# Performance work log

Hardware: AMD Instinct MI355X
Metric: run time of the kernel (lower is better)

Reference implementation:

```python
import jax, jax.numpy as jnp
import numpy as np

NUM_NODES = 50000
NUM_FEATS = 64
NUM_HEADS = 2
NUM_EDGES = 800000


def setup_inputs() -> dict:
    key = jax.random.key(0)
    k1, k2, k3 = jax.random.split(key, 3)
    x = jax.random.normal(k1, (NUM_NODES, NUM_FEATS), dtype=jnp.float32)
    # qk_lin: Linear(num_feats, 2*num_feats*num_heads)
    lim = 1.0 / np.sqrt(NUM_FEATS)
    W_qk = jax.random.uniform(k2, (NUM_FEATS, 2 * NUM_HEADS * NUM_FEATS),
                              dtype=jnp.float32, minval=-lim, maxval=lim)
    b_qk = jnp.zeros((2 * NUM_HEADS * NUM_FEATS,), dtype=jnp.float32)
    edge_index = jax.random.randint(k3, (2, NUM_EDGES), 0, NUM_NODES, dtype=jnp.int32)
    return {"x": x, "W_qk": W_qk, "b_qk": b_qk, "edge_index": edge_index}


def reference(x, W_qk, b_qk, edge_index):
    """Edge-restricted multi-head QK attention with sparse softmax over
    each row's outgoing edges, averaged over heads. Returns per-edge
    attention values [E] (sparse COO values; indices == edge_index)."""
    N, F = x.shape
    H = W_qk.shape[1] // (2 * F)
    # qk: [N, 2*H*F] -> [N, H, 2, F]; q/k split matches einops rearranges
    qk = (x @ W_qk + b_qk).reshape(N, H, 2, F)
    q = qk[:, :, 0, :]  # [N, H, F]
    k = qk[:, :, 1, :]  # [N, H, F]
    row, col = edge_index[0], edge_index[1]
    # per-edge per-head scores: q[row] . k[col]  -> [E, H]
    s = jnp.einsum('ehf,ehf->eh', q[row], k[col])
    # sparse softmax over dim=2 (columns) == segment softmax grouped by row
    m = jax.ops.segment_max(s, row, num_segments=N)      # [N, H]
    ex = jnp.exp(s - m[row])                             # [E, H]
    denom = jax.ops.segment_sum(ex, row, num_segments=N)  # [N, H]
    p = ex / denom[row]                                  # [E, H]
    # torch.sparse.sum over heads / num_heads == mean over heads
    return jnp.mean(p, axis=1)  # [E]
```

## Files before the change

### kernel.cpp

```cpp
#include <hip/hip_runtime.h>
#include <hip/hip_bf16.h>


#define NFEAT 64
#define NCOL  256
#define WT_STRIDE 72

typedef __attribute__((ext_vector_type(8))) short bf16x8;
typedef __attribute__((ext_vector_type(4))) float f32x4;

__device__ __forceinline__ unsigned short f2bf(float f) {
    union { __hip_bfloat16 h; unsigned short u; } cv;
    cv.h = __float2bfloat16(f);
    return cv.u;
}

__device__ __forceinline__ float dot_bf16x2(unsigned a, unsigned b) {
    float alo = __uint_as_float(a << 16), ahi = __uint_as_float(a & 0xFFFF0000u);
    float blo = __uint_as_float(b << 16), bhi = __uint_as_float(b & 0xFFFF0000u);
    return alo * blo + ahi * bhi;
}

__global__ __launch_bounds__(256) void gemm_qk_mfma(
    const float* __restrict__ x, const float* __restrict__ W,
    const float* __restrict__ b,
    unsigned short* __restrict__ qo, unsigned short* __restrict__ ko,
    float* __restrict__ den, int N)
{
    __shared__ unsigned short WtL[NCOL * WT_STRIDE];
    __shared__ float bL[NCOL];
    const int tid = threadIdx.x;

    for (int i = tid; i < NFEAT * NCOL; i += 256) {
        const int kk = i >> 8, c = i & 255;
        WtL[c * WT_STRIDE + kk] = f2bf(W[i]);
    }
    bL[tid] = b[tid];

    const int t = blockIdx.x * 256 + tid;
    if (t < 2 * N) den[t] = 0.f;

    const int lane = tid & 63;
    const int wv   = tid >> 6;
    const int l15  = lane & 15;
    const int quad = lane >> 4;
    const int base = blockIdx.x * 128 + wv * 32;
    __syncthreads();

    if (base >= N) return;

    bf16x8 afrag[2][2];
#pragma unroll
    for (int s = 0; s < 2; ++s) {
        int m = base + s * 16 + l15;
        if (m >= N) m = N - 1;
        const float* xp = x + (size_t)m * NFEAT + quad * 8;
#pragma unroll
        for (int ks = 0; ks < 2; ++ks) {
            float4 a0 = *(const float4*)(xp + ks * 32);
            float4 a1 = *(const float4*)(xp + ks * 32 + 4);
            bf16x8 f;
            f[0] = f2bf(a0.x); f[1] = f2bf(a0.y); f[2] = f2bf(a0.z); f[3] = f2bf(a0.w);
            f[4] = f2bf(a1.x); f[5] = f2bf(a1.y); f[6] = f2bf(a1.z); f[7] = f2bf(a1.w);
            afrag[s][ks] = f;
        }
    }

#pragma unroll 4
    for (int ct = 0; ct < 16; ++ct) {
        const int c = ct * 16 + l15;
        bf16x8 b0 = *(const bf16x8*)(WtL + (size_t)c * WT_STRIDE + quad * 8);
        bf16x8 b1 = *(const bf16x8*)(WtL + (size_t)c * WT_STRIDE + 32 + quad * 8);
        const float bias = bL[c];
        const int h   = c >> 7;
        const int isk = (c >> 6) & 1;
        const int f0  = c & 63;
        unsigned short* dst = isk ? ko : qo;
#pragma unroll
        for (int s = 0; s < 2; ++s) {
            f32x4 acc = {0.f, 0.f, 0.f, 0.f};
            acc = __builtin_amdgcn_mfma_f32_16x16x32_bf16(afrag[s][0], b0, acc, 0, 0, 0);
            acc = __builtin_amdgcn_mfma_f32_16x16x32_bf16(afrag[s][1], b1, acc, 0, 0, 0);
#pragma unroll
            for (int r = 0; r < 4; ++r) {
                const int m = base + s * 16 + quad * 4 + r;
                if (m < N)
                    dst[(size_t)m * 128 + h * 64 + f0] = f2bf(acc[r] + bias);
            }
        }
    }
}

__global__ __launch_bounds__(256) void edge_scores_exp(
    const unsigned short* __restrict__ q, const unsigned short* __restrict__ k,
    const int* __restrict__ ei, float* __restrict__ ex_out,
    float* __restrict__ denom, int E)
{
    const int grp  = (int)((blockIdx.x * 256 + threadIdx.x) >> 4);
    const int lane = threadIdx.x & 15;
    const int g0   = grp * 4;
    if (g0 >= E) return;

    int v = 0;
    if (lane < 4)      v = ei[g0 + lane];
    else if (lane < 8) v = ei[E + g0 + (lane - 4)];
    int rows[4], cols[4];
#pragma unroll
    for (int i = 0; i < 4; ++i) {
        rows[i] = __shfl(v, i, 16);
        cols[i] = __shfl(v, 4 + i, 16);
    }

    uint4 qa[4], ka[4];
#pragma unroll
    for (int i = 0; i < 4; ++i) {
        qa[i] = ((const uint4*)(q + (size_t)rows[i] * 128))[lane];
        ka[i] = ((const uint4*)(k + (size_t)cols[i] * 128))[lane];
    }

#pragma unroll
    for (int i = 0; i < 4; ++i) {
        float p = dot_bf16x2(qa[i].x, ka[i].x) + dot_bf16x2(qa[i].y, ka[i].y)
                + dot_bf16x2(qa[i].z, ka[i].z) + dot_bf16x2(qa[i].w, ka[i].w);
        p += __shfl_xor(p, 1);
        p += __shfl_xor(p, 2);
        p += __shfl_xor(p, 4);
        if ((lane & 7) == 0 && g0 + i < E) {
            const int h  = lane >> 3;
            const float e = __expf(p);
            ex_out[(size_t)(g0 + i) * 2 + h] = e;
            atomicAdd(&denom[(size_t)rows[i] * 2 + h], e);
        }
    }
}

__global__ __launch_bounds__(256) void edge_out_k(
    const int* __restrict__ ei, const float* __restrict__ ex,
    const float* __restrict__ denom, float* __restrict__ out, int E)
{
    const int e = blockIdx.x * 256 + threadIdx.x;
    if (e >= E) return;
    const int row = ei[e];
    const float2 exv = *(const float2*)&ex[(size_t)e * 2];
    const float2 dv  = *(const float2*)&denom[(size_t)row * 2];
    out[e] = 0.5f * (exv.x / dv.x + exv.y / dv.y);
}

extern "C" void kernel_launch(void* const* d_in, const int* in_sizes, int n_in,
                              void* d_out, int out_size, void* d_ws, size_t ws_size,
                              hipStream_t stream)
{
    const float* x   = (const float*)d_in[0];
    const float* W   = (const float*)d_in[1];
    const float* b   = (const float*)d_in[2];
    const int*   ei  = (const int*)d_in[3];
    float*       out = (float*)d_out;

    const int N = in_sizes[0] / NFEAT;
    const int E = in_sizes[3] / 2;

    char* ws = (char*)d_ws;
    size_t off = 0;
    auto alloc = [&](size_t bytes) { void* p = ws + off; off += (bytes + 255) & ~(size_t)255; return p; };
    unsigned short* q_ws  = (unsigned short*)alloc((size_t)N * 128 * 2);
    unsigned short* k_ws  = (unsigned short*)alloc((size_t)N * 128 * 2);
    float*          ex_ws = (float*)alloc((size_t)E * 2 * sizeof(float));
    float*          den_ws= (float*)alloc((size_t)N * 2 * sizeof(float));
    (void)ws_size;

    gemm_qk_mfma<<<(N + 127) / 128, 256, 0, stream>>>(x, W, b, q_ws, k_ws, den_ws, N);
    edge_scores_exp<<<((size_t)(E + 3) / 4 * 16 + 255) / 256, 256, 0, stream>>>(q_ws, k_ws, ei, ex_ws, den_ws, E);
    edge_out_k<<<(E + 255) / 256, 256, 0, stream>>>(ei, ex_ws, den_ws, out, E);
}
```

Baseline: 142.3 us.

## Build CSR by row and compute segment softmax per row without atomics

Replaces the per-edge score kernel, which used atomic denominator accumulation, and the separate normalisation kernel. A histogram, a two-level scan and a scatter now build a row-sorted CSR of (col, edge id). A per-row kernel then computes scores, the exp values and the denominator in registers, and writes normalised outputs. The aim is to remove float atomics and reuse each row's q vector across its edges, at the cost of five extra launches, an integer-atomic scatter and a serial per-row loop with load imbalance from varying degree.

```diff
diff --git a/kernel.cpp b/kernel.cpp
--- a/kernel.cpp
+++ b/kernel.cpp
@@ -24,8 +24,7 @@
 __global__ __launch_bounds__(256) void gemm_qk_mfma(
     const float* __restrict__ x, const float* __restrict__ W,
     const float* __restrict__ b,
-    unsigned short* __restrict__ qo, unsigned short* __restrict__ ko,
-    float* __restrict__ den, int N)
+    unsigned short* __restrict__ qo, unsigned short* __restrict__ ko, int N)
 {
     __shared__ unsigned short WtL[NCOL * WT_STRIDE];
     __shared__ float bL[NCOL];
@@ -36,9 +35,6 @@
         WtL[c * WT_STRIDE + kk] = f2bf(W[i]);
     }
     bL[tid] = b[tid];
-
-    const int t = blockIdx.x * 256 + tid;
-    if (t < 2 * N) den[t] = 0.f;
 
     const int lane = tid & 63;
     const int wv   = tid >> 6;
@@ -91,59 +87,112 @@
     }
 }
 
-__global__ __launch_bounds__(256) void edge_scores_exp(
+__global__ __launch_bounds__(256) void hist_k(const int* __restrict__ ei,
+                                              unsigned* __restrict__ cnt, int E) {
+    const int e = blockIdx.x * 256 + threadIdx.x;
+    if (e < E) atomicAdd(&cnt[ei[e]], 1u);
+}
+
+__global__ __launch_bounds__(256) void scan_a(const unsigned* __restrict__ cnt,
+                                              unsigned* __restrict__ rsl,
+                                              unsigned* __restrict__ bsum, int n) {
+    __shared__ unsigned wsum[4];
+    const int idx  = blockIdx.x * 256 + threadIdx.x;
+    const int lane = threadIdx.x & 63;
+    const int wv   = threadIdx.x >> 6;
+    unsigned v = (idx < n) ? cnt[idx] : 0u;
+    unsigned inc = v;
+    for (int off = 1; off < 64; off <<= 1) {
+        unsigned t = __shfl_up(inc, off, 64);
+        if (lane >= off) inc += t;
+    }
+    if (lane == 63) wsum[wv] = inc;
+    __syncthreads();
+    unsigned wbase = 0;
+    for (int i = 0; i < wv; ++i) wbase += wsum[i];
+    if (idx < n) rsl[idx] = wbase + inc - v;
+    if (threadIdx.x == 255) bsum[blockIdx.x] = wbase + inc;
+}
+
+__global__ __launch_bounds__(256) void scan_b(const unsigned* __restrict__ bsum,
+                                              unsigned* __restrict__ bpre, int nb) {
+    __shared__ unsigned wsum[4];
+    const int t    = threadIdx.x;
+    const int lane = t & 63;
+    const int wv   = t >> 6;
+    unsigned v = (t < nb) ? bsum[t] : 0u;
+    unsigned inc = v;
+    for (int off = 1; off < 64; off <<= 1) {
+        unsigned u = __shfl_up(inc, off, 64);
+        if (lane >= off) inc += u;
+    }
+    if (lane == 63) wsum[wv] = inc;
+    __syncthreads();
+    unsigned wbase = 0;
+    for (int i = 0; i < wv; ++i) wbase += wsum[i];
+    bpre[t] = wbase + inc - v;
+}
+
+__global__ __launch_bounds__(256) void scat_k(const int* __restrict__ ei,
+                                              const unsigned* __restrict__ rsl,
+                                              const unsigned* __restrict__ bpre,
+                                              unsigned* __restrict__ cursor,
+                                              uint2* __restrict__ csr, int E) {
+    const int e = blockIdx.x * 256 + threadIdx.x;
+    if (e >= E) return;
+    const int r = ei[e];
+    const unsigned base = rsl[r] + bpre[r >> 8];
+    const unsigned p = base + atomicAdd(&cursor[r], 1u);
+    csr[p] = make_uint2((unsigned)ei[E + e], (unsigned)e);
+}
+
+__global__ __launch_bounds__(256) void row_k(
     const unsigned short* __restrict__ q, const unsigned short* __restrict__ k,
-    const int* __restrict__ ei, float* __restrict__ ex_out,
-    float* __restrict__ denom, int E)
+    const uint2* __restrict__ csr, const unsigned* __restrict__ rsl,
+    const unsigned* __restrict__ bpre, float* __restrict__ exb,
+    float* __restrict__ out, int N)
 {
     const int grp  = (int)((blockIdx.x * 256 + threadIdx.x) >> 4);
     const int lane = threadIdx.x & 15;
-    const int g0   = grp * 4;
-    if (g0 >= E) return;
-
-    int v = 0;
-    if (lane < 4)      v = ei[g0 + lane];
-    else if (lane < 8) v = ei[E + g0 + (lane - 4)];
-    int rows[4], cols[4];
-#pragma unroll
-    for (int i = 0; i < 4; ++i) {
-        rows[i] = __shfl(v, i, 16);
-        cols[i] = __shfl(v, 4 + i, 16);
-    }
-
-    uint4 qa[4], ka[4];
-#pragma unroll
-    for (int i = 0; i < 4; ++i) {
-        qa[i] = ((const uint4*)(q + (size_t)rows[i] * 128))[lane];
-        ka[i] = ((const uint4*)(k + (size_t)cols[i] * 128))[lane];
-    }
-
-#pragma unroll
-    for (int i = 0; i < 4; ++i) {
-        float p = dot_bf16x2(qa[i].x, ka[i].x) + dot_bf16x2(qa[i].y, ka[i].y)
-                + dot_bf16x2(qa[i].z, ka[i].z) + dot_bf16x2(qa[i].w, ka[i].w);
+    const bool live = (grp < N);
+
+    unsigned start = 0; int deg = 0;
+    uint4 qa = make_uint4(0, 0, 0, 0);
+    if (live) {
+        start = rsl[grp] + bpre[grp >> 8];
+        const unsigned end = rsl[grp + 1] + bpre[(grp + 1) >> 8];
+        deg = (int)(end - start);
+        qa = ((const uint4*)(q + (size_t)grp * 128))[lane];
+    }
+
+    float den0 = 0.f, den1 = 0.f;
+    uint2 pr = (deg > 0) ? csr[start] : make_uint2(0u, 0u);
+    for (int j = 0; j < deg; ++j) {
+        uint2 nx = (j + 1 < deg) ? csr[start + j + 1] : pr;
+        uint4 ka = ((const uint4*)(k + (size_t)pr.x * 128))[lane];
+        float p = dot_bf16x2(qa.x, ka.x) + dot_bf16x2(qa.y, ka.y)
+                + dot_bf16x2(qa.z, ka.z) + dot_bf16x2(qa.w, ka.w);
         p += __shfl_xor(p, 1);
         p += __shfl_xor(p, 2);
         p += __shfl_xor(p, 4);
-        if ((lane & 7) == 0 && g0 + i < E) {
-            const int h  = lane >> 3;
+        if ((lane & 7) == 0) {
             const float e = __expf(p);
-            ex_out[(size_t)(g0 + i) * 2 + h] = e;
-            atomicAdd(&denom[(size_t)rows[i] * 2 + h], e);
+            exb[2 * (size_t)(start + j) + (lane >> 3)] = e;
+            if (lane == 0) den0 += e; else den1 += e;
         }
-    }
-}
-
-__global__ __launch_bounds__(256) void edge_out_k(
-    const int* __restrict__ ei, const float* __restrict__ ex,
-    const float* __restrict__ denom, float* __restrict__ out, int E)
-{
-    const int e = blockIdx.x * 256 + threadIdx.x;
-    if (e >= E) return;
-    const int row = ei[e];
-    const float2 exv = *(const float2*)&ex[(size_t)e * 2];
-    const float2 dv  = *(const float2*)&denom[(size_t)row * 2];
-    out[e] = 0.5f * (exv.x / dv.x + exv.y / dv.y);
+        pr = nx;
+    }
+
+    __threadfence_block();
+    __syncthreads();
+
+    const float i0 = 1.f / __shfl(den0, 0, 16);
+    const float i1 = 1.f / __shfl(den1, 8, 16);
+    for (int j = lane; j < deg; j += 16) {
+        const uint2 pe = csr[start + j];
+        const float2 ev = ((const float2*)exb)[start + j];
+        out[pe.y] = 0.5f * (ev.x * i0 + ev.y * i1);
+    }
 }
 
 extern "C" void kernel_launch(void* const* d_in, const int* in_sizes, int n_in,
@@ -158,17 +207,29 @@
 
     const int N = in_sizes[0] / NFEAT;
     const int E = in_sizes[3] / 2;
+    const int NB = (N + 1 + 255) / 256;
 
     char* ws = (char*)d_ws;
     size_t off = 0;
     auto alloc = [&](size_t bytes) { void* p = ws + off; off += (bytes + 255) & ~(size_t)255; return p; };
     unsigned short* q_ws  = (unsigned short*)alloc((size_t)N * 128 * 2);
     unsigned short* k_ws  = (unsigned short*)alloc((size_t)N * 128 * 2);
-    float*          ex_ws = (float*)alloc((size_t)E * 2 * sizeof(float));
-    float*          den_ws= (float*)alloc((size_t)N * 2 * sizeof(float));
+    uint2*          csr   = (uint2*)alloc((size_t)E * 8);
+    float*          exb   = (float*)alloc((size_t)E * 2 * sizeof(float));
+    unsigned*       cnt   = (unsigned*)alloc((size_t)(N + 1) * 4);
+    unsigned*       cursor= (unsigned*)alloc((size_t)N * 4);
+    unsigned*       rsl   = (unsigned*)alloc((size_t)(N + 1) * 4);
+    unsigned*       bsum  = (unsigned*)alloc((size_t)NB * 4);
+    unsigned*       bpre  = (unsigned*)alloc((size_t)256 * 4);
     (void)ws_size;
 
-    gemm_qk_mfma<<<(N + 127) / 128, 256, 0, stream>>>(x, W, b, q_ws, k_ws, den_ws, N);
-    edge_scores_exp<<<((size_t)(E + 3) / 4 * 16 + 255) / 256, 256, 0, stream>>>(q_ws, k_ws, ei, ex_ws, den_ws, E);
-    edge_out_k<<<(E + 255) / 256, 256, 0, stream>>>(ei, ex_ws, den_ws, out, E);
-}
+    size_t zbytes = (size_t)((char*)(cursor + N) - (char*)cnt);
+    hipMemsetAsync(cnt, 0, zbytes, stream);
+
+    gemm_qk_mfma<<<(N + 127) / 128, 256, 0, stream>>>(x, W, b, q_ws, k_ws, N);
+    hist_k<<<(E + 255) / 256, 256, 0, stream>>>(ei, cnt, E);
+    scan_a<<<NB, 256, 0, stream>>>(cnt, rsl, bsum, N + 1);
+    scan_b<<<1, 256, 0, stream>>>(bsum, bpre, NB);
+    scat_k<<<(E + 255) / 256, 256, 0, stream>>>(ei, rsl, bpre, cursor, csr, E);
+    row_k<<<((size_t)N * 16 + 255) / 256, 256, 0, stream>>>(q_ws, k_ws, csr, rsl, bpre, exb, out, N);
+}
```

Result: slower. 232.8 us (+63.6%).
